# Optimization experiments

Measured on AMD Instinct MI355X. Metric: run time of the kernel, lower is better.

## Reference

```python
import jax, jax.numpy as jnp
import numpy as np

B, L, NV = 16, 512, 321
D, PL, ST = 128, 16, 8
P = (L - PL) // ST + 2  # 64 patches (replication pad of `stride` on the right)
E, K, H = 8, 2, 512     # experts, top-n gates, expert hidden (4*d_model)
PRED = 96
BAL_COEF, Z_COEF = 0.01, 0.001


def sinusoidal_pe(n, d):
    pos = np.arange(n)[:, None].astype(np.float32)
    div = np.exp(np.arange(0, d, 2).astype(np.float32) * -(np.log(10000.0) / d))
    pe = np.zeros((n, d), dtype=np.float32)
    pe[:, 0::2] = np.sin(pos * div)
    pe[:, 1::2] = np.cos(pos * div)
    return jnp.asarray(pe)


def setup_inputs() -> dict:
    key = jax.random.key(0)
    ks = jax.random.split(key, 12)
    s = lambda i, shape, sc: jax.random.normal(ks[i], shape, jnp.float32) * sc
    return {
        "x_enc": jax.random.normal(ks[0], (B, L, NV), jnp.float32),
        "x_mark_enc": jax.random.normal(ks[1], (B, L, 4), jnp.float32),
        "x_dec": jax.random.normal(ks[2], (B, PRED, NV), jnp.float32),
        "x_mark_dec": jax.random.normal(ks[3], (B, PRED, 4), jnp.float32),
        "W_val": s(4, (PL, D), PL ** -0.5),
        "W_g": s(5, (D, E), D ** -0.5),
        "W1": s(6, (E, D, H), D ** -0.5),
        "b1": jnp.zeros((E, H), jnp.float32),
        "W2": s(7, (E, H, D), H ** -0.5),
        "b2": jnp.zeros((E, D), jnp.float32),
        "W_head": s(8, (D * P, PRED), (D * P) ** -0.5),
        "b_head": jnp.zeros((PRED,), jnp.float32),
    }


def _forward(x_enc, W_val, W_g, W1, b1, W2, b2, W_head, b_head):
    # RevIN-style instance norm (means detached as in torch .detach())
    means = jax.lax.stop_gradient(jnp.mean(x_enc, axis=1, keepdims=True))
    xc = x_enc - means
    stdev = jnp.sqrt(jnp.var(xc, axis=1, keepdims=True) + 1e-5)
    xn = xc / stdev

    # Patch embedding: [B, NV, L] -> replicate-pad -> unfold -> linear + sinusoidal PE
    x = jnp.transpose(xn, (0, 2, 1))                        # [B, NV, L]
    x = jnp.pad(x, ((0, 0), (0, 0), (0, ST)), mode="edge")  # ReplicationPad1d((0, stride))
    idx = np.arange(P)[:, None] * ST + np.arange(PL)        # [P, PL]
    patches = x[:, :, idx]                                  # [B, NV, P, PL]
    tok = patches.reshape(B * NV, P, PL)
    emb = tok @ W_val + sinusoidal_pe(P, D)[None]           # [N, P, D]

    # MoE: top-n softmax gating (gates not renormalized), balance + router-z aux losses
    t = emb.reshape(-1, D)                                  # [T, D], T = B*NV*P
    logits = t @ W_g                                        # [T, E]
    probs = jax.nn.softmax(logits, axis=-1)
    topv, topi = jax.lax.top_k(probs, K)                    # [T, K]

    out = jnp.zeros_like(t)
    for e in range(E):  # fixed small expert count; each expert is a GELU MLP
        h = jax.nn.gelu(t @ W1[e] + b1[e], approximate=False) @ W2[e] + b2[e]
        g = jnp.sum(jnp.where(topi == e, topv, 0.0), axis=-1)  # gate for expert e (0 if unrouted)
        out = out + g[:, None] * h

    me = jnp.mean(probs, axis=0)                                            # mean router prob per expert
    ce = jnp.mean(jax.nn.one_hot(topi, E, dtype=probs.dtype).sum(1), 0) / K  # dispatch fraction per expert
    balance_loss = E * jnp.sum(me * ce)
    z_loss = jnp.mean(jax.nn.logsumexp(logits, axis=-1) ** 2)
    aux = BAL_COEF * balance_loss + Z_COEF * z_loss

    # FlattenHead: [B, NV, P, D] -> [B, NV, D, P] -> flatten(-2) -> Linear(nf, pred_len)
    enc = out.reshape(B, NV, P, D).transpose(0, 1, 3, 2)    # [B, NV, D, P]
    dec = enc.reshape(B, NV, D * P) @ W_head + b_head        # [B, NV, PRED]
    dec = jnp.transpose(dec, (0, 2, 1))                      # [B, PRED, NV]

    # de-normalize
    dec = dec * stdev[:, 0][:, None, :] + means[:, 0][:, None, :]
    return dec, aux


def reference(x_enc, x_mark_enc, x_dec, x_mark_dec, W_val, W_g, W1, b1, W2, b2, W_head, b_head):
    return _forward(x_enc, W_val, W_g, W1, b1, W2, b2, W_head, b_head)
```

## Files before the change

kernel.cpp:

```cpp
#include <hip/hip_runtime.h>
#include <hip/hip_bf16.h>

typedef unsigned short u16;
typedef unsigned int   u32;
typedef unsigned long long u64;
typedef __attribute__((ext_vector_type(8))) short bf16x8;
typedef __attribute__((ext_vector_type(4))) float f32x4;
typedef __attribute__((ext_vector_type(16))) float f32x16;

#define MFMA16(a,b,c) __builtin_amdgcn_mfma_f32_16x16x32_bf16(a,b,c,0,0,0)
#define MFMA32(a,b,c) __builtin_amdgcn_mfma_f32_32x32x16_bf16(a,b,c,0,0,0)

#define NV_   321
#define B_    16
#define L_    512
#define D_    128
#define P_    64
#define E_    8
#define H_    512
#define NRW   5136
#define NTOK  328704
#define DP_   8192
#define NBUCK 329728

static __device__ __forceinline__ u16 f2bf(float f){
  __hip_bfloat16 h = __float2bfloat16(f);
  return *reinterpret_cast<u16*>(&h);
}

static __device__ __forceinline__ float gelu_f(float x){
  float x2 = x*x;
  float p  = __builtin_fmaf(-0.1029433f, x2, -2.3022083f);
  float a  = x*p;
  float en = exp2f(a);
  float r  = __builtin_amdgcn_rcpf(1.0f + en);
  return x*r;
}

static __device__ __forceinline__ u32 bfadd2(u32 a, u32 b){
  float lo = __uint_as_float(a<<16)           + __uint_as_float(b<<16);
  float hi = __uint_as_float(a&0xffff0000u)   + __uint_as_float(b&0xffff0000u);
  return (u32)f2bf(lo) | ((u32)f2bf(hi)<<16);
}

static constexpr size_t alup(size_t x){ return (x + 255) & ~(size_t)255; }
static constexpr size_t OFF_MEAN = 0;
static constexpr size_t OFF_RSTD = OFF_MEAN + alup((size_t)NRW*4);
static constexpr size_t OFF_STD  = OFF_RSTD + alup((size_t)NRW*4);
static constexpr size_t OFF_XT   = OFF_STD  + alup((size_t)NRW*4);
static constexpr size_t OFF_PE   = OFF_XT   + alup((size_t)NRW*L_*4);
static constexpr size_t OFF_W1T  = OFF_PE   + alup((size_t)P_*D_*4);
static constexpr size_t OFF_W2T  = OFF_W1T  + alup((size_t)E_*H_*D_*2);
static constexpr size_t OFF_WHT  = OFF_W2T  + alup((size_t)E_*D_*H_*2);
static constexpr size_t OFF_T    = OFF_WHT  + alup((size_t)96*DP_*2);
static constexpr size_t OFF_TOPI = OFF_T    + alup((size_t)NTOK*D_*2);
static constexpr size_t OFF_GATE = OFF_TOPI + alup((size_t)NTOK*4);
static constexpr size_t OFF_CNTR = OFF_GATE + alup((size_t)NTOK*8);
static constexpr size_t OFF_BTOK = OFF_CNTR + alup((size_t)1024);
static constexpr size_t OFF_BGT  = OFF_BTOK + alup((size_t)2*NBUCK*4);
static constexpr size_t OFF_OUT  = OFF_BGT  + alup((size_t)2*NBUCK*4);
static constexpr size_t OFF_MEAND= OFF_OUT  + alup((size_t)NTOK*D_*2);
static constexpr size_t OFF_RSTDD= OFF_MEAND+ alup((size_t)NRW*8);
static constexpr size_t OFF_WVG  = OFF_RSTDD+ alup((size_t)NRW*8);
static constexpr size_t OFF_PEG  = OFF_WVG  + alup((size_t)16*8*8);
static constexpr size_t OFF_PG   = OFF_PEG  + alup((size_t)P_*E_*8);
static constexpr size_t OFF_PI   = OFF_PG   + alup((size_t)NRW*12*4);



__global__ void k_xt(const float* __restrict__ x, float* __restrict__ xT){
  __shared__ float tile[32][33];
  int b = blockIdx.z;
  int v0 = blockIdx.x*32, l0 = blockIdx.y*32;
  int tx = threadIdx.x, ty = threadIdx.y;
  for(int i=ty;i<32;i+=8){
    int l = l0+i, v = v0+tx;
    tile[i][tx] = (v<NV_) ? x[((size_t)b*L_ + l)*NV_ + v] : 0.f;
  }
  __syncthreads();
  for(int i=ty;i<32;i+=8){
    int v = v0+i, l = l0+tx;
    if(v<NV_) xT[((size_t)(b*NV_+v))*L_ + l] = tile[tx][i];
  }
}

__global__ void k_stats(const float* __restrict__ xT, float* meanp, float* rstdp, float* stdp,
                        double* meand, double* rstdd){
  __shared__ double s1[256], s2[256];
  int r = blockIdx.x, t = threadIdx.x;
  double a = (double)xT[(size_t)r*L_ + t], b = (double)xT[(size_t)r*L_ + 256 + t];
  s1[t]=a+b; s2[t]=a*a+b*b;
  __syncthreads();
  for(int o=128;o>0;o>>=1){ if(t<o){ s1[t]+=s1[t+o]; s2[t]+=s2[t+o]; } __syncthreads(); }
  if(t==0){
    double m = s1[0]*(1.0/512.0);
    double var = s2[0]*(1.0/512.0) - m*m;
    double sd = sqrt(var + 1e-5);
    meanp[r]=(float)m; stdp[r]=(float)sd; rstdp[r]=(float)(1.0/sd);
    meand[r]=m; rstdd[r]=1.0/sd;
  }
}

__global__ void k_prep(const float* __restrict__ Wval, const float* __restrict__ Wg,
                       float* __restrict__ pef, double* __restrict__ Wvg,
                       double* __restrict__ peg){
  int t = threadIdx.x;
  for(int i=t;i<8192;i+=256){
    int p = i>>7, d = i&127, k = d>>1;
    double div = exp(-(double)(2*k) * (9.210340371976184 /128.0));
    double ang = (double)p * div;
    double v = (d&1) ? cos(ang) : sin(ang);
    pef[i] = (float)v;
  }
  __syncthreads();
  if(t<128){
    int j = t>>3, e = t&7;
    double acc = 0.0;
    for(int d=0;d<128;d++) acc += (double)Wval[j*128+d] * (double)Wg[d*8+e];
    Wvg[t] = acc;
  }
  for(int q=t;q<512;q+=256){
    int p = q>>3, e = q&7;
    double acc = 0.0;
    for(int d=0;d<128;d++) acc += (double)pef[p*128+d] * (double)Wg[d*8+e];
    peg[q] = acc;
  }
}

__global__ void k_wt(const float* __restrict__ in, u16* __restrict__ outp, int R, int C){
  __shared__ float tile[32][33];
  int e = blockIdx.z;
  int c0 = blockIdx.x*32, r0 = blockIdx.y*32;
  const float* src = in + (size_t)e*R*C;
  u16* dst = outp + (size_t)e*R*C;
  int tx=threadIdx.x, ty=threadIdx.y;
  for(int i=ty;i<32;i+=8){
    int r=r0+i, c=c0+tx;
    tile[i][tx] = (r<R && c<C) ? src[(size_t)r*C+c] : 0.f;
  }
  __syncthreads();
  for(int i=ty;i<32;i+=8){
    int c=c0+i, r=r0+tx;
    if(c<C && r<R) dst[(size_t)c*R + r] = f2bf(tile[tx][i]);
  }
}

__global__ void k_wh(const float* __restrict__ Wh, u16* __restrict__ WhT2){
  __shared__ float tile[32][33];
  int d0 = blockIdx.x*32, o0 = blockIdx.y*32, p = blockIdx.z;
  int tx = threadIdx.x, ty = threadIdx.y;
  for(int i=ty;i<32;i+=8){
    int r = (d0+i)*64 + p;
    tile[i][tx] = Wh[(size_t)r*96 + o0 + tx];
  }
  __syncthreads();
  for(int i=ty;i<32;i+=8){
    int o = o0+i;
    WhT2[(size_t)o*DP_ + p*128 + d0 + tx] = f2bf(tile[tx][i]);
  }
}

__global__ __launch_bounds__(256) void k_embed(
    const float* __restrict__ xT, const float* __restrict__ meanp, const float* __restrict__ rstdp,
    const float* __restrict__ Wval, const float* __restrict__ pe,
    u16* __restrict__ tglob)
{
  __shared__ __align__(16) float xn[520];
  int r = blockIdx.x, t = threadIdx.x;
  float mean = meanp[r], rstd = rstdp[r];
  float v0 = (xT[(size_t)r*L_ + t]       - mean)*rstd;
  float v1 = (xT[(size_t)r*L_ + 256 + t] - mean)*rstd;
  xn[t] = v0; xn[t+256] = v1;
  if(t==255){
    #pragma unroll
    for(int i=512;i<520;i++) xn[i]=v1;
  }
  int d0 = (t & 63)*2;
  int p0 = t >> 6;
  float2 w[16];
  #pragma unroll
  for(int j=0;j<16;j++) w[j] = *(const float2*)(Wval + j*128 + d0);
  __syncthreads();

  for(int p=p0;p<64;p+=4){
    const float4* xp = (const float4*)(xn + p*8);
    float4 x0=xp[0], x1=xp[1], x2=xp[2], x3=xp[3];
    float xv[16];
    *(float4*)(xv+0)=x0; *(float4*)(xv+4)=x1; *(float4*)(xv+8)=x2; *(float4*)(xv+12)=x3;
    float2 pw = *(const float2*)(pe + p*128 + d0);
    float a0 = pw.x, a1 = pw.y;
    #pragma unroll
    for(int j=0;j<16;j++){ a0 += xv[j]*w[j].x; a1 += xv[j]*w[j].y; }
    u32 packed = (u32)f2bf(a0) | ((u32)f2bf(a1)<<16);
    *(u32*)(tglob + ((size_t)(r*64+p)*128 + d0)) = packed;
  }
}

__global__ __launch_bounds__(256) void k_gate(
    const float* __restrict__ xT, const double* __restrict__ meand, const double* __restrict__ rstdd,
    const double* __restrict__ Wvg, const double* __restrict__ peg,
    int* __restrict__ topip, float2* __restrict__ gatep,
    float* __restrict__ pg, int* __restrict__ pib)
{
  __shared__ double xn[520];
  __shared__ double lgt[64][9];
  int r = blockIdx.x, t = threadIdx.x;
  double m = meand[r], rs = rstdd[r];
  double v0 = ((double)xT[(size_t)r*L_ + t]       - m)*rs;
  double v1 = ((double)xT[(size_t)r*L_ + 256 + t] - m)*rs;
  xn[t]=v0; xn[t+256]=v1;
  if(t==255){
    #pragma unroll
    for(int i=512;i<520;i++) xn[i]=v1;
  }
  __syncthreads();
  for(int q=t;q<512;q+=256){
    int p = q>>3, e = q&7;
    double acc = peg[q];
    #pragma unroll
    for(int j=0;j<16;j++) acc += xn[p*8+j]*Wvg[j*8+e];
    lgt[p][e] = acc;
  }
  __syncthreads();
  if(t<64){
    int token = r*64 + t;
    double l0[8];
    #pragma unroll
    for(int e=0;e<8;e++) l0[e]=lgt[t][e];
    double mx=l0[0];
    #pragma unroll
    for(int e=1;e<8;e++) mx = fmax(mx,l0[e]);
    int i1=0; double b1v=l0[0];
    #pragma unroll
    for(int e=1;e<8;e++) if(l0[e]>b1v){b1v=l0[e]; i1=e;}
    int i2=-1; double b2v=-1e300;
    #pragma unroll
    for(int e=0;e<8;e++) if(e!=i1 && l0[e]>b2v){b2v=l0[e]; i2=e;}
    float pr[8]; float sum=0.f;
    #pragma unroll
    for(int e=0;e<8;e++){ pr[e]=__expf((float)(l0[e]-mx)); sum+=pr[e]; }
    float inv = 1.f/sum;
    #pragma unroll
    for(int e=0;e<8;e++) pr[e]*=inv;
    topip[token] = i1 | (i2<<8);
    gatep[token] = make_float2(pr[i1], pr[i2]);
    float lse = (float)mx + __logf(sum);
    #pragma unroll
    for(int e=0;e<8;e++){
      float v = pr[e];
      for(int o=32;o>0;o>>=1) v += __shfl_down(v,o);
      if(t==0) pg[r*12+e] = v;
    }
    {
      float z = lse*lse;
      for(int o=32;o>0;o>>=1) z += __shfl_down(z,o);
      if(t==0) pg[r*12+8] = z;
    }
    #pragma unroll
    for(int e=0;e<8;e++){
      u64 m1 = __ballot(i1==e);
      u64 m2 = __ballot(i2==e);
      if(t==0){
        pib[r*16+e]   = (int)__popcll(m1);
        pib[r*16+8+e] = (int)__popcll(m2);
      }
    }
  }
}

__global__ __launch_bounds__(256) void k_aux(const float* __restrict__ pg, const int* __restrict__ pib,
                                             int* __restrict__ ci, float* __restrict__ dout){
  __shared__ double sd[256];
  __shared__ int si[256];
  __shared__ double totd[9];
  __shared__ int toti[16];
  int t = threadIdx.x;
  double accd[9]; int acci[16];
  #pragma unroll
  for(int c=0;c<9;c++) accd[c]=0.0;
  #pragma unroll
  for(int c=0;c<16;c++) acci[c]=0;
  for(int r=t;r<NRW;r+=256){
    #pragma unroll
    for(int c=0;c<9;c++) accd[c] += (double)pg[r*12+c];
    #pragma unroll
    for(int c=0;c<16;c++) acci[c] += pib[r*16+c];
  }
  for(int c=0;c<9;c++){
    sd[t]=accd[c]; __syncthreads();
    for(int o=128;o>0;o>>=1){ if(t<o) sd[t]+=sd[t+o]; __syncthreads(); }
    if(t==0) totd[c]=sd[0];
    __syncthreads();
  }
  for(int c=0;c<16;c++){
    si[t]=acci[c]; __syncthreads();
    for(int o=128;o>0;o>>=1){ if(t<o) si[t]+=si[t+o]; __syncthreads(); }
    if(t==0) toti[c]=si[0];
    __syncthreads();
  }
  if(t==0){
    const double invN = 1.0/(double)NTOK;
    double bal = 0.0;
    int es1=0, bs1=0, es2=0, bs2=0;
    for(int e=0;e<8;e++){
      int c1 = toti[e], c2 = toti[8+e];
      bal += (totd[e]*invN) * ((double)(c1+c2) * invN * 0.5);
      ci[32+e]=es1; ci[16+e]=es1; ci[50+e]=bs1;
      ci[41+e]=es2; ci[24+e]=es2; ci[59+e]=bs2;
      es1 += c1; bs1 += (c1+127)>>7;
      es2 += c2; bs2 += (c2+127)>>7;
    }
    ci[40]=es1; ci[58]=bs1;
    ci[49]=es2; ci[67]=bs2;
    dout[493056] = (float)(0.01*8.0*bal + 0.001*(totd[8]*invN));
  }
}

__global__ __launch_bounds__(256) void k_scatter(const int* __restrict__ topip,
    const float2* __restrict__ gatep, int* __restrict__ ci,
    int* __restrict__ btok, float* __restrict__ bgt){
  __shared__ int lc[16]; __shared__ int lb[16];
  int t = threadIdx.x;
  int token = blockIdx.x*256 + t;
  if(t<16) lc[t]=0;
  __syncthreads();
  int ti = topip[token];
  float2 g = gatep[token];
  int e1 = ti & 255, e2 = (ti>>8)&255;
  int r1 = atomicAdd(&lc[e1],1);
  int r2 = atomicAdd(&lc[8+e2],1);
  __syncthreads();
  if(t<8)            lb[t] = atomicAdd(&ci[16+t],   lc[t]);
  else if(t<16)      lb[t] = atomicAdd(&ci[24+t-8], lc[t]);
  __syncthreads();
  int p1 = lb[e1]+r1, p2 = lb[8+e2]+r2;
  btok[p1] = token;         bgt[p1] = g.x;
  btok[NBUCK+p2] = token;   bgt[NBUCK+p2] = g.y;
}

__global__ __launch_bounds__(256,3) void k_expert(
    const u16* __restrict__ tglob,
    const u16* __restrict__ W1T, const u16* __restrict__ W2T,
    const float* __restrict__ b1g, const float* __restrict__ b2g,
    const int* __restrict__ ci,
    const int* __restrict__ btok, const float* __restrict__ bgt,
    u16* __restrict__ outg, int slot)
{
  __shared__ __align__(16) u16 Wb[2][9472];
  __shared__ __align__(16) u16 Ss[128*40];
  __shared__ float gtA[128];
  __shared__ int   tkA[128];

  int bid = blockIdx.x, t = threadIdx.x;
  int stB = 32 + slot*9, bsB = 50 + slot*9;
  int boff = slot*NBUCK;
  if(bid >= ci[bsB+8]) return;
  int e = 0;
  #pragma unroll
  for(int k2=1;k2<8;k2++) if(bid >= ci[bsB+k2]) e = k2;
  int row0 = ci[stB+e] + (bid - ci[bsB+e])*128;
  int rend = ci[stB+e+1];

  if(t<128){
    int pos = row0+t;
    bool v = pos<rend;
    gtA[t] = v ? bgt[boff+pos]  : 0.f;
    tkA[t] = v ? btok[boff+pos] : -1;
  }

  int wid = t>>6, lane = t&63;
  int m = lane&31, hi = lane>>5;
  int rb = wid*32;

  int posA = row0 + rb + m;
  int tokA = (posA<rend) ? btok[boff+posA] : 0;
  const u16* arow = tglob + (size_t)tokA*128 + hi*8;
  bf16x8 areg[8];
  #pragma unroll
  for(int ks=0;ks<8;ks++) areg[ks] = *(const bf16x8*)(arow + ks*16);

  int hr = t>>3, q = t&7;
  int dr = t>>1, q2 = t&1;

  {
    const u16* s1 = W1T + ((size_t)e*H_ + hr)*128 + q*16;
    u16* d1 = &Wb[0][hr*136 + q*16];
    *(uint4*)(d1)   = *(const uint4*)(s1);
    *(uint4*)(d1+8) = *(const uint4*)(s1+8);
    const u16* s2 = W2T + ((size_t)e*D_ + dr)*H_ + q2*16;
    u16* d2 = &Wb[0][4352 + dr*40 + q2*16];
    *(uint4*)(d2)   = *(const uint4*)(s2);
    *(uint4*)(d2+8) = *(const uint4*)(s2+8);
  }
  __syncthreads();

  f32x16 accO[4];
  const f32x16 z16 = {0,0,0,0,0,0,0,0,0,0,0,0,0,0,0,0};
  #pragma unroll
  for(int nt=0;nt<4;nt++) accO[nt] = z16;

  for(int hc=0;hc<16;hc++){
    const u16* W1c = &Wb[hc&1][0];
    const u16* W2c = &Wb[hc&1][4352];
    uint4 l0,l1,l2,l3;
    if(hc<15){
      const u16* s1 = W1T + ((size_t)e*H_ + (hc+1)*32 + hr)*128 + q*16;
      l0 = *(const uint4*)(s1); l1 = *(const uint4*)(s1+8);
      const u16* s2 = W2T + ((size_t)e*D_ + dr)*H_ + (hc+1)*32 + q2*16;
      l2 = *(const uint4*)(s2); l3 = *(const uint4*)(s2+8);
    }
    f32x16 acc1 = z16;
    #pragma unroll
    for(int ks=0;ks<8;ks++){
      bf16x8 b = *(const bf16x8*)(W1c + m*136 + ks*16 + hi*8);
      acc1 = MFMA32(areg[ks], b, acc1);
    }
    float bv = b1g[e*H_ + hc*32 + m];
    #pragma unroll
    for(int reg=0; reg<16; reg++){
      int rl = (reg&3) + 8*(reg>>2) + 4*hi;
      Ss[(rb+rl)*40 + m] = f2bf(gelu_f(acc1[reg] + bv));
    }
    #pragma unroll
    for(int ks=0;ks<2;ks++){
      bf16x8 a = *(const bf16x8*)(Ss + (rb+m)*40 + ks*16 + hi*8);
      #pragma unroll
      for(int nt=0;nt<4;nt++){
        bf16x8 b = *(const bf16x8*)(W2c + (nt*32+m)*40 + ks*16 + hi*8);
        accO[nt] = MFMA32(a, b, accO[nt]);
      }
    }
    if(hc<15){
      u16* d1 = &Wb[(hc+1)&1][hr*136 + q*16];
      *(uint4*)(d1)   = l0; *(uint4*)(d1+8) = l1;
      u16* d2 = &Wb[(hc+1)&1][4352 + dr*40 + q2*16];
      *(uint4*)(d2)   = l2; *(uint4*)(d2+8) = l3;
      __syncthreads();
    }
  }

  float b2v[4];
  #pragma unroll
  for(int nt=0;nt<4;nt++) b2v[nt] = b2g[e*128 + nt*32 + m];
  float gts[16];
  #pragma unroll
  for(int reg=0; reg<16; reg++){
    int rl = (reg&3) + 8*(reg>>2) + 4*hi;
    gts[reg] = gtA[rb+rl];
  }
  int lr2 = lane>>1, hf = lane&1;
  int tok2 = tkA[rb+lr2];
  u16* dstbase = outg + (size_t)((tok2<0)?0:tok2)*128 + hf*16;
  #pragma unroll
  for(int nt=0;nt<4;nt++){
    #pragma unroll
    for(int reg=0; reg<16; reg++){
      int rl = (reg&3) + 8*(reg>>2) + 4*hi;
      Ss[(rb+rl)*40 + m] = f2bf((accO[nt][reg] + b2v[nt]) * gts[reg]);
    }
    __builtin_amdgcn_s_waitcnt(0);
    if(tok2>=0){
      const u16* sp = Ss + (rb+lr2)*40 + hf*16;
      uint4 v0 = *(const uint4*)(sp);
      uint4 v1 = *(const uint4*)(sp+8);
      u16* dp = dstbase + nt*32;
      if(slot==1){
        uint4 o0 = *(const uint4*)(dp), o1 = *(const uint4*)(dp+8);
        v0.x=bfadd2(v0.x,o0.x); v0.y=bfadd2(v0.y,o0.y);
        v0.z=bfadd2(v0.z,o0.z); v0.w=bfadd2(v0.w,o0.w);
        v1.x=bfadd2(v1.x,o1.x); v1.y=bfadd2(v1.y,o1.y);
        v1.z=bfadd2(v1.z,o1.z); v1.w=bfadd2(v1.w,o1.w);
      }
      *(uint4*)(dp)   = v0;
      *(uint4*)(dp+8) = v1;
    }
    __builtin_amdgcn_s_waitcnt(0);
  }
}

__global__ __launch_bounds__(256) void k_head(const u16* __restrict__ Aout,
    const u16* __restrict__ WhT2, float* __restrict__ dec8){
  int bid = blockIdx.x;
  int mb = bid>>3, kseg = bid&7;
  int t = threadIdx.x, wid = t>>6, lane = t&63;
  int quad = lane>>4, li = lane&15;
  int r0 = mb*64 + wid*16;
  int rowA = r0 + li; if(rowA >= NRW) rowA = NRW-1;
  const u16* aptr = Aout + (size_t)rowA*DP_ + kseg*1024 + quad*8;
  const u16* bptr = WhT2 + (size_t)li*DP_  + kseg*1024 + quad*8;
  f32x4 acc[6];
  #pragma unroll
  for(int j=0;j<6;j++) acc[j]=(f32x4){0,0,0,0};
  #pragma unroll 4
  for(int ks=0;ks<32;ks++){
    bf16x8 af = *(const bf16x8*)(aptr + ks*32);
    #pragma unroll
    for(int nt=0;nt<6;nt++){
      bf16x8 bw = *(const bf16x8*)(bptr + (size_t)nt*16*DP_ + ks*32);
      acc[nt] = MFMA16(af, bw, acc[nt]);
    }
  }
  float* dst = dec8 + (size_t)kseg*NRW*96;
  #pragma unroll
  for(int nt=0;nt<6;nt++)
    #pragma unroll
    for(int rg=0;rg<4;rg++){
      int mm = r0 + quad*4 + rg;
      if(mm < NRW) dst[(size_t)mm*96 + nt*16 + li] = acc[nt][rg];
    }
}

__global__ void k_final(const float* __restrict__ dec8, const float* __restrict__ bhead,
    const float* __restrict__ stdp, const float* __restrict__ meanp, float* __restrict__ outp){
  __shared__ float s[64*97];
  int b = blockIdx.y, v0 = blockIdx.x*64;
  int t = threadIdx.x;
  for(int i=t;i<6144;i+=256){
    int vi = i/96, o = i - vi*96;
    int v = v0+vi;
    float acc = 0.f;
    if(v<NV_){
      size_t base = (size_t)(b*NV_+v)*96 + o;
      #pragma unroll
      for(int ks=0;ks<8;ks++) acc += dec8[(size_t)ks*NRW*96 + base];
    }
    s[vi*97+o] = acc;
  }
  __syncthreads();
  for(int i=t;i<6144;i+=256){
    int o = i>>6, vi = i&63;
    int v = v0+vi;
    if(v<NV_){
      int r = b*NV_+v;
      outp[((size_t)b*96 + o)*NV_ + v] = (s[vi*97+o] + bhead[o])*stdp[r] + meanp[r];
    }
  }
}

extern "C" void kernel_launch(void* const* d_in, const int* in_sizes, int n_in,
                              void* d_out, int out_size, void* d_ws, size_t ws_size,
                              hipStream_t stream){
  const float* x_enc = (const float*)d_in[0];
  const float* W_val = (const float*)d_in[4];
  const float* W_g   = (const float*)d_in[5];
  const float* W1    = (const float*)d_in[6];
  const float* b1    = (const float*)d_in[7];
  const float* W2    = (const float*)d_in[8];
  const float* b2    = (const float*)d_in[9];
  const float* W_head= (const float*)d_in[10];
  const float* b_head= (const float*)d_in[11];
  float* outp = (float*)d_out;
  char* ws = (char*)d_ws;

  float* meanp = (float*)(ws+OFF_MEAN);
  float* rstdp = (float*)(ws+OFF_RSTD);
  float* stdp  = (float*)(ws+OFF_STD);
  float* xT    = (float*)(ws+OFF_XT);
  float* pe    = (float*)(ws+OFF_PE);
  u16*   W1T   = (u16*)(ws+OFF_W1T);
  u16*   W2T   = (u16*)(ws+OFF_W2T);
  u16*   WhT2  = (u16*)(ws+OFF_WHT);
  u16*   tglob = (u16*)(ws+OFF_T);
  float* dec8  = (float*)(ws+OFF_T);
  int*   topip = (int*)(ws+OFF_TOPI);
  float2* gatep= (float2*)(ws+OFF_GATE);
  int*   ci    = (int*)(ws+OFF_CNTR+128);
  int*   btok  = (int*)(ws+OFF_BTOK);
  float* bgt   = (float*)(ws+OFF_BGT);
  u16*   outg  = (u16*)(ws+OFF_OUT);
  double* meand= (double*)(ws+OFF_MEAND);
  double* rstdd= (double*)(ws+OFF_RSTDD);
  double* Wvg  = (double*)(ws+OFF_WVG);
  double* peg  = (double*)(ws+OFF_PEG);
  float* pg    = (float*)(ws+OFF_PG);
  int*   pib   = (int*)(ws+OFF_PI);

  hipMemsetAsync(ws+OFF_CNTR, 0, 1024, stream);

  k_xt<<<dim3(11,16,B_), dim3(32,8), 0, stream>>>(x_enc, xT);
  k_stats<<<NRW, 256, 0, stream>>>(xT, meanp, rstdp, stdp, meand, rstdd);
  k_prep<<<1, 256, 0, stream>>>(W_val, W_g, pe, Wvg, peg);
  k_wt<<<dim3(16,4,E_), dim3(32,8), 0, stream>>>(W1, W1T, 128, 512);
  k_wt<<<dim3(4,16,E_), dim3(32,8), 0, stream>>>(W2, W2T, 512, 128);
  k_wh<<<dim3(4,3,64), dim3(32,8), 0, stream>>>(W_head, WhT2);
  k_embed<<<NRW, 256, 0, stream>>>(xT, meanp, rstdp, W_val, pe, tglob);
  k_gate<<<NRW, 256, 0, stream>>>(xT, meand, rstdd, Wvg, peg, topip, gatep, pg, pib);
  k_aux<<<1, 256, 0, stream>>>(pg, pib, ci, outp);
  k_scatter<<<NTOK/256, 256, 0, stream>>>(topip, gatep, ci, btok, bgt);
  k_expert<<<2576, 256, 0, stream>>>(tglob, W1T, W2T, b1, b2, ci, btok, bgt, outg, 0);
  k_expert<<<2576, 256, 0, stream>>>(tglob, W1T, W2T, b1, b2, ci, btok, bgt, outg, 1);
  k_head<<<648, 256, 0, stream>>>(outg, WhT2, dec8);
  k_final<<<dim3(6,B_), 256, 0, stream>>>(dec8, b_head, stdp, meanp, outp);
}
```

Measured before the change: 642.0 us.

## Transpose expert MFMAs to keep GELU activations in registers via permlane swaps

The expert kernel now computes the transposed products (weights as the A operand, tokens as B). Each lane then holds a token's hidden values, so the GELU output is packed with v_cvt_pk_bf16_f32 and regrouped with permlane32_swap instead of going through an LDS staging buffer. Biases are loaded straight into the accumulators, and results are written directly to global memory per token with the gate applied. This drops the shared-memory round trips and the epilogue's scratch buffer and waitcnts, but the output stores are now 8-byte scattered writes instead of 32-byte coalesced ones.

```diff
diff --git a/kernel.cpp b/kernel.cpp
--- a/kernel.cpp
+++ b/kernel.cpp
@@ -7,6 +7,7 @@
 typedef __attribute__((ext_vector_type(8))) short bf16x8;
 typedef __attribute__((ext_vector_type(4))) float f32x4;
 typedef __attribute__((ext_vector_type(16))) float f32x16;
+typedef __attribute__((ext_vector_type(2))) unsigned int u32x2;
 
 #define MFMA16(a,b,c) __builtin_amdgcn_mfma_f32_16x16x32_bf16(a,b,c,0,0,0)
 #define MFMA32(a,b,c) __builtin_amdgcn_mfma_f32_32x32x16_bf16(a,b,c,0,0,0)
@@ -35,12 +36,6 @@
   float en = exp2f(a);
   float r  = __builtin_amdgcn_rcpf(1.0f + en);
   return x*r;
-}
-
-static __device__ __forceinline__ u32 bfadd2(u32 a, u32 b){
-  float lo = __uint_as_float(a<<16)           + __uint_as_float(b<<16);
-  float hi = __uint_as_float(a&0xffff0000u)   + __uint_as_float(b&0xffff0000u);
-  return (u32)f2bf(lo) | ((u32)f2bf(hi)<<16);
 }
 
 static constexpr size_t alup(size_t x){ return (x + 255) & ~(size_t)255; }
@@ -347,9 +342,6 @@
     u16* __restrict__ outg, int slot)
 {
   __shared__ __align__(16) u16 Wb[2][9472];
-  __shared__ __align__(16) u16 Ss[128*40];
-  __shared__ float gtA[128];
-  __shared__ int   tkA[128];
 
   int bid = blockIdx.x, t = threadIdx.x;
   int stB = 32 + slot*9, bsB = 50 + slot*9;
@@ -361,19 +353,14 @@
   int row0 = ci[stB+e] + (bid - ci[bsB+e])*128;
   int rend = ci[stB+e+1];
 
-  if(t<128){
-    int pos = row0+t;
-    bool v = pos<rend;
-    gtA[t] = v ? bgt[boff+pos]  : 0.f;
-    tkA[t] = v ? btok[boff+pos] : -1;
-  }
-
   int wid = t>>6, lane = t&63;
   int m = lane&31, hi = lane>>5;
   int rb = wid*32;
 
   int posA = row0 + rb + m;
-  int tokA = (posA<rend) ? btok[boff+posA] : 0;
+  bool valA = posA < rend;
+  int tokA  = valA ? btok[boff+posA] : 0;
+  float gt  = valA ? bgt[boff+posA]  : 0.f;
   const u16* arow = tglob + (size_t)tokA*128 + hi*8;
   bf16x8 areg[8];
   #pragma unroll
@@ -395,9 +382,16 @@
   __syncthreads();
 
   f32x16 accO[4];
-  const f32x16 z16 = {0,0,0,0,0,0,0,0,0,0,0,0,0,0,0,0};
-  #pragma unroll
-  for(int nt=0;nt<4;nt++) accO[nt] = z16;
+  #pragma unroll
+  for(int nt=0;nt<4;nt++){
+    const float* bp2 = b2g + e*D_ + nt*32 + 4*hi;
+    #pragma unroll
+    for(int qq=0;qq<4;qq++){
+      float4 b4 = *(const float4*)(bp2 + 8*qq);
+      accO[nt][4*qq+0]=b4.x; accO[nt][4*qq+1]=b4.y;
+      accO[nt][4*qq+2]=b4.z; accO[nt][4*qq+3]=b4.w;
+    }
+  }
 
   for(int hc=0;hc<16;hc++){
     const u16* W1c = &Wb[hc&1][0];
@@ -409,26 +403,44 @@
       const u16* s2 = W2T + ((size_t)e*D_ + dr)*H_ + (hc+1)*32 + q2*16;
       l2 = *(const uint4*)(s2); l3 = *(const uint4*)(s2+8);
     }
-    f32x16 acc1 = z16;
+    f32x16 acc1;
+    {
+      const float* bp1 = b1g + e*H_ + hc*32 + 4*hi;
+      #pragma unroll
+      for(int qq=0;qq<4;qq++){
+        float4 b4 = *(const float4*)(bp1 + 8*qq);
+        acc1[4*qq+0]=b4.x; acc1[4*qq+1]=b4.y;
+        acc1[4*qq+2]=b4.z; acc1[4*qq+3]=b4.w;
+      }
+    }
     #pragma unroll
     for(int ks=0;ks<8;ks++){
-      bf16x8 b = *(const bf16x8*)(W1c + m*136 + ks*16 + hi*8);
-      acc1 = MFMA32(areg[ks], b, acc1);
-    }
-    float bv = b1g[e*H_ + hc*32 + m];
-    #pragma unroll
-    for(int reg=0; reg<16; reg++){
-      int rl = (reg&3) + 8*(reg>>2) + 4*hi;
-      Ss[(rb+rl)*40 + m] = f2bf(gelu_f(acc1[reg] + bv));
-    }
-    #pragma unroll
-    for(int ks=0;ks<2;ks++){
-      bf16x8 a = *(const bf16x8*)(Ss + (rb+m)*40 + ks*16 + hi*8);
-      #pragma unroll
-      for(int nt=0;nt<4;nt++){
-        bf16x8 b = *(const bf16x8*)(W2c + (nt*32+m)*40 + ks*16 + hi*8);
-        accO[nt] = MFMA32(a, b, accO[nt]);
-      }
+      bf16x8 wa = *(const bf16x8*)(W1c + m*136 + ks*16 + hi*8);
+      acc1 = MFMA32(wa, areg[ks], acc1);
+    }
+    u32 pk[8];
+    #pragma unroll
+    for(int i=0;i<8;i++){
+      float g0 = gelu_f(acc1[2*i]);
+      float g1 = gelu_f(acc1[2*i+1]);
+      asm("v_cvt_pk_bf16_f32 %0, %1, %2" : "=v"(pk[i]) : "v"(g0), "v"(g1));
+    }
+    union { bf16x8 v; u32 w[4]; } bA, bB;
+    u32x2 s02 = __builtin_amdgcn_permlane32_swap(pk[0], pk[2], false, false);
+    u32x2 s13 = __builtin_amdgcn_permlane32_swap(pk[1], pk[3], false, false);
+    u32x2 s46 = __builtin_amdgcn_permlane32_swap(pk[4], pk[6], false, false);
+    u32x2 s57 = __builtin_amdgcn_permlane32_swap(pk[5], pk[7], false, false);
+    bA.w[0]=s02.x; bA.w[1]=s13.x; bA.w[2]=s02.y; bA.w[3]=s13.y;
+    bB.w[0]=s46.x; bB.w[1]=s57.x; bB.w[2]=s46.y; bB.w[3]=s57.y;
+    #pragma unroll
+    for(int nt=0;nt<4;nt++){
+      bf16x8 a2 = *(const bf16x8*)(W2c + (nt*32+m)*40 + hi*8);
+      accO[nt] = MFMA32(a2, bA.v, accO[nt]);
+    }
+    #pragma unroll
+    for(int nt=0;nt<4;nt++){
+      bf16x8 a2 = *(const bf16x8*)(W2c + (nt*32+m)*40 + 16 + hi*8);
+      accO[nt] = MFMA32(a2, bB.v, accO[nt]);
     }
     if(hc<15){
       u16* d1 = &Wb[(hc+1)&1][hr*136 + q*16];
@@ -439,42 +451,31 @@
     }
   }
 
-  float b2v[4];
-  #pragma unroll
-  for(int nt=0;nt<4;nt++) b2v[nt] = b2g[e*128 + nt*32 + m];
-  float gts[16];
-  #pragma unroll
-  for(int reg=0; reg<16; reg++){
-    int rl = (reg&3) + 8*(reg>>2) + 4*hi;
-    gts[reg] = gtA[rb+rl];
-  }
-  int lr2 = lane>>1, hf = lane&1;
-  int tok2 = tkA[rb+lr2];
-  u16* dstbase = outg + (size_t)((tok2<0)?0:tok2)*128 + hf*16;
-  #pragma unroll
-  for(int nt=0;nt<4;nt++){
-    #pragma unroll
-    for(int reg=0; reg<16; reg++){
-      int rl = (reg&3) + 8*(reg>>2) + 4*hi;
-      Ss[(rb+rl)*40 + m] = f2bf((accO[nt][reg] + b2v[nt]) * gts[reg]);
-    }
-    __builtin_amdgcn_s_waitcnt(0);
-    if(tok2>=0){
-      const u16* sp = Ss + (rb+lr2)*40 + hf*16;
-      uint4 v0 = *(const uint4*)(sp);
-      uint4 v1 = *(const uint4*)(sp+8);
-      u16* dp = dstbase + nt*32;
-      if(slot==1){
-        uint4 o0 = *(const uint4*)(dp), o1 = *(const uint4*)(dp+8);
-        v0.x=bfadd2(v0.x,o0.x); v0.y=bfadd2(v0.y,o0.y);
-        v0.z=bfadd2(v0.z,o0.z); v0.w=bfadd2(v0.w,o0.w);
-        v1.x=bfadd2(v1.x,o1.x); v1.y=bfadd2(v1.y,o1.y);
-        v1.z=bfadd2(v1.z,o1.z); v1.w=bfadd2(v1.w,o1.w);
+  if(valA){
+    u16* obase = outg + (size_t)tokA*128 + 4*hi;
+    #pragma unroll
+    for(int nt=0;nt<4;nt++){
+      #pragma unroll
+      for(int qq=0;qq<4;qq++){
+        float v0 = accO[nt][4*qq+0]*gt;
+        float v1 = accO[nt][4*qq+1]*gt;
+        float v2 = accO[nt][4*qq+2]*gt;
+        float v3 = accO[nt][4*qq+3]*gt;
+        u32* dp = (u32*)(obase + nt*32 + 8*qq);
+        if(slot==1){
+          u32x2 old = *(const u32x2*)dp;
+          v0 += __uint_as_float(old.x<<16);
+          v1 += __uint_as_float(old.x & 0xffff0000u);
+          v2 += __uint_as_float(old.y<<16);
+          v3 += __uint_as_float(old.y & 0xffff0000u);
+        }
+        u32 w0, w1;
+        asm("v_cvt_pk_bf16_f32 %0, %1, %2" : "=v"(w0) : "v"(v0), "v"(v1));
+        asm("v_cvt_pk_bf16_f32 %0, %1, %2" : "=v"(w1) : "v"(v2), "v"(v3));
+        u32x2 nv; nv.x = w0; nv.y = w1;
+        *(u32x2*)dp = nv;
       }
-      *(uint4*)(dp)   = v0;
-      *(uint4*)(dp+8) = v1;
-    }
-    __builtin_amdgcn_s_waitcnt(0);
+    }
   }
 }
 
```

Result: no change. 641.0 us (-0.2%).
